# Kernel optimization log

Measured on AMD Instinct MI355X. Metric: run time of the kernel, lower is better.

Reference implementation:

```python
import jax, jax.numpy as jnp
import numpy as np

N = 100000
E = 1600000
IN, H, OUT = 128, 128, 64


def setup_inputs() -> dict:
    key = jax.random.key(0)
    k1, k2, k3, k4, k5, k6 = jax.random.split(key, 6)
    x = jax.random.normal(k1, (N, IN), dtype=jnp.float32)
    edge_index = jax.random.randint(k2, (2, E), 0, N, dtype=jnp.int64)
    W1 = jax.random.normal(k3, (IN, H), dtype=jnp.float32) / np.sqrt(IN)
    b1 = jnp.zeros((H,), dtype=jnp.float32)
    W2 = jax.random.normal(k4, (H, OUT), dtype=jnp.float32) / np.sqrt(H)
    b2 = jnp.zeros((OUT,), dtype=jnp.float32)
    return {"x": x, "edge_index": edge_index, "W1": W1, "b1": b1, "W2": W2, "b2": b2}


def gcn_conv(x, src, dst, W, b, num_nodes):
    # PyG GCNConv: linear transform, then symmetric-normalized aggregation
    h = x @ W                                         # (N, d_out)
    ones = jnp.ones(src.shape[0], dtype=h.dtype)
    deg = jax.ops.segment_sum(ones, dst, num_segments=num_nodes)  # in-degree incl. self-loops
    dis = jax.lax.rsqrt(jnp.maximum(deg, 1.0))        # deg >= 1 due to self-loops
    norm = dis[src] * dis[dst]                        # (E+N,)
    msg = h[src] * norm[:, None]                      # gather + scale (memory-bound)
    out = jax.ops.segment_sum(msg, dst, num_segments=num_nodes)
    return out + b


def reference(x, edge_index, W1, b1, W2, b2):
    loop = jnp.arange(N, dtype=edge_index.dtype)
    src = jnp.concatenate([edge_index[0], loop])
    dst = jnp.concatenate([edge_index[1], loop])
    h = gcn_conv(x, src, dst, W1, b1, N)
    h = jax.nn.relu(h)                                # dropout: eval mode (identity)
    out = gcn_conv(h, src, dst, W2, b2, N)
    return jax.nn.sigmoid(out) * 0.8 + 0.1
```

## Files before the change

kernel.cpp:

```cpp
#include <hip/hip_runtime.h>
#include <cstdint>
#include <cstddef>

#define IN_F 128
#define HID  128
#define OUTF 64

typedef unsigned int   uint32;
typedef unsigned short ushort16;

using frag_ab = __attribute__((ext_vector_type(8))) short;
using frag_cd = __attribute__((ext_vector_type(4))) float;

static constexpr int TPB = 256;
static constexpr int PT_TILE = 2048;
static constexpr int PT_EPT  = 8;
static constexpr int MAXBK   = 512;

__device__ __forceinline__ float bflo(uint32 u) { return __uint_as_float(u << 16); }
__device__ __forceinline__ float bfhi(uint32 u) { return __uint_as_float(u & 0xFFFF0000u); }
__device__ __forceinline__ ushort16 f2bf(float f) {
    uint32 x = __float_as_uint(f);
    x = (x + 0x7FFFu + ((x >> 16) & 1u)) >> 16;
    return (ushort16)x;
}
__device__ __forceinline__ uint32 packbf(float a, float b) {
    return (uint32)f2bf(a) | ((uint32)f2bf(b) << 16);
}

__global__ void detect_i64_kernel(const uint32* __restrict__ p, int npairs, int* __restrict__ flag) {
    __shared__ int anynz;
    if (threadIdx.x == 0) anynz = 0;
    __syncthreads();
    int i = threadIdx.x;
    if (i < npairs && p[2 * i + 1] != 0u) atomicOr(&anynz, 1);
    __syncthreads();
    if (threadIdx.x == 0) *flag = (anynz == 0) ? 1 : 0;
}

__device__ __forceinline__ int load_idx(const void* p, int i, bool i64) {
    return i64 ? (int)((const long long*)p)[i] : ((const int*)p)[i];
}

__global__ __launch_bounds__(256) void partition_kernel(
    const void* __restrict__ ei, int E, const int* __restrict__ flag,
    int nbuckets, int bcap,
    int* __restrict__ bcur, uint32* __restrict__ bbuf)
{
    __shared__ uint32   stash[PT_TILE];
    __shared__ ushort16 bidx[PT_TILE];
    __shared__ int hist[MAXBK];
    __shared__ int scanb[MAXBK];
    __shared__ int gbase[MAXBK];
    __shared__ int sum256[256];

    bool i64 = (*flag != 0);
    int tile0 = blockIdx.x * PT_TILE;
    int tid = threadIdx.x;

    for (int i = tid; i < nbuckets; i += 256) hist[i] = 0;
    __syncthreads();

    uint32 pck[PT_EPT];
    int    lofs[PT_EPT];
    short  bkt[PT_EPT];
#pragma unroll
    for (int j = 0; j < PT_EPT; ++j) {
        int e = tile0 + j * 256 + tid;
        if (e < E) {
            int s = load_idx(ei, e, i64);
            int d = load_idx(ei, E + e, i64);
            int b = d >> 8;
            pck[j]  = (uint32)s | ((uint32)(d & 255) << 24);
            bkt[j]  = (short)b;
            lofs[j] = atomicAdd(&hist[b], 1);
        } else bkt[j] = -1;
    }
    __syncthreads();

    for (int i = tid; i < nbuckets; i += 256)
        gbase[i] = hist[i] ? atomicAdd(&bcur[i], hist[i]) : 0;

    {
        int lt = tid * 2;
        int h0 = 0, h1 = 0;
        if (lt + 0 < nbuckets) h0 = hist[lt + 0];
        if (lt + 1 < nbuckets) h1 = hist[lt + 1];
        int lsum = h0 + h1;
        sum256[tid] = lsum;
        __syncthreads();
        for (int off = 1; off < 256; off <<= 1) {
            int t = (tid >= off) ? sum256[tid - off] : 0;
            __syncthreads();
            sum256[tid] += t;
            __syncthreads();
        }
        int excl = sum256[tid] - lsum;
        if (lt + 0 < nbuckets) scanb[lt + 0] = excl;
        if (lt + 1 < nbuckets) scanb[lt + 1] = excl + h0;
    }
    __syncthreads();

#pragma unroll
    for (int j = 0; j < PT_EPT; ++j) {
        if (bkt[j] >= 0) {
            int p = scanb[bkt[j]] + lofs[j];
            stash[p] = pck[j];
            bidx[p]  = (ushort16)bkt[j];
        }
    }
    __syncthreads();

    int total = min(PT_TILE, E - tile0);
    for (int k = tid; k < total; k += 256) {
        int b = bidx[k];
        int dst = gbase[b] + (k - scanb[b]);
        if (dst < bcap) bbuf[(size_t)b * bcap + dst] = stash[k];
    }
}

__global__ __launch_bounds__(256) void bucket_count_kernel(
    const uint32* __restrict__ bbuf, const int* __restrict__ bcur,
    int* __restrict__ counts, float* __restrict__ dis, int N, int bcap)
{
    __shared__ int h[256];
    int tid = threadIdx.x;
    h[tid] = 0;
    __syncthreads();
    int b = blockIdx.x;
    int cnt = min(bcur[b], bcap);
    const uint32* src = bbuf + (size_t)b * bcap;
    for (int k = tid; k < cnt; k += 256) atomicAdd(&h[src[k] >> 24], 1);
    __syncthreads();
    int node = (b << 8) + tid;
    if (node < N) {
        int c = h[tid];
        counts[node] = c;
        dis[node] = rsqrtf((float)(c + 1));
    }
}

__global__ __launch_bounds__(256) void bucket_fill_kernel(
    const uint32* __restrict__ bbuf, const int* __restrict__ bcur,
    const int* __restrict__ row_ptr, int* __restrict__ csr, int N, int bcap)
{
    __shared__ int cur[256];
    int b = blockIdx.x;
    int node = (b << 8) + threadIdx.x;
    cur[threadIdx.x] = (node < N) ? row_ptr[node] : 0;
    __syncthreads();
    int cnt = min(bcur[b], bcap);
    const uint32* src = bbuf + (size_t)b * bcap;
    for (int k = threadIdx.x; k < cnt; k += 256) {
        uint32 p = src[k];
        int dl = p >> 24;
        int pos = atomicAdd(&cur[dl], 1);
        csr[pos] = (int)(p & 0xFFFFFF);
    }
}

__global__ void hist_kernel(const void* __restrict__ ei, int E, const int* __restrict__ flag,
                            int* __restrict__ counts) {
    int e = blockIdx.x * TPB + threadIdx.x;
    if (e >= E) return;
    bool i64 = (*flag != 0);
    atomicAdd(&counts[load_idx(ei, E + e, i64)], 1);
}

__global__ void fill_kernel(const void* __restrict__ ei, int E, const int* __restrict__ flag,
                            int* __restrict__ cursor, int* __restrict__ csr_src) {
    int e = blockIdx.x * TPB + threadIdx.x;
    if (e >= E) return;
    bool i64 = (*flag != 0);
    int s = load_idx(ei, e, i64);
    int d = load_idx(ei, E + e, i64);
    int pos = atomicAdd(&cursor[d], 1);
    csr_src[pos] = s;
}

__global__ void dis_kernel(const int* __restrict__ counts, float* __restrict__ dis, int n) {
    int i = blockIdx.x * TPB + threadIdx.x;
    if (i < n) dis[i] = rsqrtf((float)(counts[i] + 1));
}

__global__ void scan_block_kernel(const int* __restrict__ counts, int* __restrict__ excl,
                                  int* __restrict__ partials, int n) {
    __shared__ int tmp[TPB];
    int tid = threadIdx.x, gid = blockIdx.x * TPB + tid;
    int v = (gid < n) ? counts[gid] : 0;
    tmp[tid] = v;
    __syncthreads();
    for (int off = 1; off < TPB; off <<= 1) {
        int t = (tid >= off) ? tmp[tid - off] : 0;
        __syncthreads();
        tmp[tid] += t;
        __syncthreads();
    }
    if (gid < n) excl[gid] = tmp[tid] - v;
    if (tid == TPB - 1) partials[blockIdx.x] = tmp[TPB - 1];
}

__global__ void scan_partials_kernel(int* __restrict__ partials, int nb) {
    __shared__ int tmp[512];
    int tid = threadIdx.x;
    int v = (tid < nb) ? partials[tid] : 0;
    tmp[tid] = v;
    __syncthreads();
    for (int off = 1; off < 512; off <<= 1) {
        int t = (tid >= off) ? tmp[tid - off] : 0;
        __syncthreads();
        tmp[tid] += t;
        __syncthreads();
    }
    if (tid < nb) partials[tid] = tmp[tid] - v;
}

__global__ void add_offsets_kernel(int* __restrict__ excl, const int* __restrict__ partials,
                                   int* __restrict__ cursor, int n) {
    int i = blockIdx.x * TPB + threadIdx.x;
    if (i < n) {
        int v = excl[i] + partials[blockIdx.x];
        excl[i] = v;
        cursor[i] = v;
    }
}

template <int C, bool XBF>
__global__ __launch_bounds__(256) void gemm_mfma_kernel(
    const void* __restrict__ Xv, const float* __restrict__ W,
    const float* __restrict__ dis, ushort16* __restrict__ out, int M)
{
    constexpr int NB = C / 16;
    __shared__ ushort16 Wt[C][136];

    for (int i = threadIdx.x; i < 128 * C; i += 256) {
        int k = i / C, c = i % C;
        Wt[c][k] = f2bf(W[i]);
    }
    __syncthreads();

    int wid  = threadIdx.x >> 6;
    int lane = threadIdx.x & 63;
    int g    = lane >> 4;
    int li   = lane & 15;

    int row = blockIdx.x * 64 + wid * 16 + li;
    int rc  = min(row, M - 1);

    frag_cd acc[NB];
#pragma unroll
    for (int i = 0; i < NB; ++i) acc[i] = (frag_cd)0.0f;

#pragma unroll
    for (int t = 0; t < 4; ++t) {
        frag_ab a;
        if (XBF) {
            const ushort16* xp = (const ushort16*)Xv + (size_t)rc * 128 + t * 32 + g * 8;
            a = *(const frag_ab*)xp;
        } else {
            const float* xp = (const float*)Xv + (size_t)rc * 128 + t * 32 + g * 8;
            float4 p = *(const float4*)xp;
            float4 q = *(const float4*)(xp + 4);
            a[0] = (short)f2bf(p.x); a[1] = (short)f2bf(p.y);
            a[2] = (short)f2bf(p.z); a[3] = (short)f2bf(p.w);
            a[4] = (short)f2bf(q.x); a[5] = (short)f2bf(q.y);
            a[6] = (short)f2bf(q.z); a[7] = (short)f2bf(q.w);
        }
#pragma unroll
        for (int cb = 0; cb < NB; ++cb) {
            frag_ab b = *(const frag_ab*)&Wt[cb * 16 + li][t * 32 + g * 8];
            acc[cb] = __builtin_amdgcn_mfma_f32_16x16x32_bf16(a, b, acc[cb], 0, 0, 0);
        }
    }

    int ro = blockIdx.x * 64 + wid * 16 + g * 4;
#pragma unroll
    for (int r = 0; r < 4; ++r) {
        int rr = ro + r;
        if (rr < M) {
            float dsc = dis[rr];
#pragma unroll
            for (int cb = 0; cb < NB; ++cb)
                out[(size_t)rr * C + cb * 16 + li] = f2bf(acc[cb][r] * dsc);
        }
    }
}

__global__ __launch_bounds__(256) void agg128_kernel(
    const uint32* __restrict__ hs, const int* __restrict__ csr,
    const int* __restrict__ row_ptr, const int* __restrict__ counts,
    const float* __restrict__ dis, const float* __restrict__ b,
    uint32* __restrict__ out, int n)
{
    int wave = threadIdx.x >> 6;
    int lane = threadIdx.x & 63;
    int g    = lane >> 4;
    int sl   = lane & 15;
    int node = blockIdx.x * 4 + wave;
    if (node >= n) return;

    const uint4* hsv = (const uint4*)hs;
    float a0 = 0.f, a1 = 0.f, a2 = 0.f, a3 = 0.f,
          a4 = 0.f, a5 = 0.f, a6 = 0.f, a7 = 0.f;
    if (g == 0) {
        uint4 u = hsv[(size_t)node * 16 + sl];
        a0 = bflo(u.x); a1 = bfhi(u.x); a2 = bflo(u.y); a3 = bfhi(u.y);
        a4 = bflo(u.z); a5 = bfhi(u.z); a6 = bflo(u.w); a7 = bfhi(u.w);
    }

    int start = row_ptr[node];
    int end   = start + counts[node];
    int k = start;
    for (; k + 15 < end; k += 16) {
        int base = k + (g << 2);
        int s0 = csr[base], s1 = csr[base + 1], s2 = csr[base + 2], s3 = csr[base + 3];
        uint4 u0 = hsv[(size_t)s0 * 16 + sl];
        uint4 u1 = hsv[(size_t)s1 * 16 + sl];
        uint4 u2 = hsv[(size_t)s2 * 16 + sl];
        uint4 u3 = hsv[(size_t)s3 * 16 + sl];
        a0 += bflo(u0.x) + bflo(u1.x) + bflo(u2.x) + bflo(u3.x);
        a1 += bfhi(u0.x) + bfhi(u1.x) + bfhi(u2.x) + bfhi(u3.x);
        a2 += bflo(u0.y) + bflo(u1.y) + bflo(u2.y) + bflo(u3.y);
        a3 += bfhi(u0.y) + bfhi(u1.y) + bfhi(u2.y) + bfhi(u3.y);
        a4 += bflo(u0.z) + bflo(u1.z) + bflo(u2.z) + bflo(u3.z);
        a5 += bfhi(u0.z) + bfhi(u1.z) + bfhi(u2.z) + bfhi(u3.z);
        a6 += bflo(u0.w) + bflo(u1.w) + bflo(u2.w) + bflo(u3.w);
        a7 += bfhi(u0.w) + bfhi(u1.w) + bfhi(u2.w) + bfhi(u3.w);
    }
    for (; k + 7 < end; k += 8) {
        int base = k + (g << 1);
        int s0 = csr[base], s1 = csr[base + 1];
        uint4 u0 = hsv[(size_t)s0 * 16 + sl];
        uint4 u1 = hsv[(size_t)s1 * 16 + sl];
        a0 += bflo(u0.x) + bflo(u1.x);  a1 += bfhi(u0.x) + bfhi(u1.x);
        a2 += bflo(u0.y) + bflo(u1.y);  a3 += bfhi(u0.y) + bfhi(u1.y);
        a4 += bflo(u0.z) + bflo(u1.z);  a5 += bfhi(u0.z) + bfhi(u1.z);
        a6 += bflo(u0.w) + bflo(u1.w);  a7 += bfhi(u0.w) + bfhi(u1.w);
    }
    for (; k < end; k += 4) {
        int e = k + g;
        if (e < end) {
            uint4 u = hsv[(size_t)csr[e] * 16 + sl];
            a0 += bflo(u.x); a1 += bfhi(u.x); a2 += bflo(u.y); a3 += bfhi(u.y);
            a4 += bflo(u.z); a5 += bfhi(u.z); a6 += bflo(u.w); a7 += bfhi(u.w);
        }
    }

    a0 += __shfl_xor(a0, 16, 64); a0 += __shfl_xor(a0, 32, 64);
    a1 += __shfl_xor(a1, 16, 64); a1 += __shfl_xor(a1, 32, 64);
    a2 += __shfl_xor(a2, 16, 64); a2 += __shfl_xor(a2, 32, 64);
    a3 += __shfl_xor(a3, 16, 64); a3 += __shfl_xor(a3, 32, 64);
    a4 += __shfl_xor(a4, 16, 64); a4 += __shfl_xor(a4, 32, 64);
    a5 += __shfl_xor(a5, 16, 64); a5 += __shfl_xor(a5, 32, 64);
    a6 += __shfl_xor(a6, 16, 64); a6 += __shfl_xor(a6, 32, 64);
    a7 += __shfl_xor(a7, 16, 64); a7 += __shfl_xor(a7, 32, 64);

    if (g == 0) {
        float dsc = dis[node];
        float4 bb0 = ((const float4*)b)[sl * 2];
        float4 bb1 = ((const float4*)b)[sl * 2 + 1];
        float v0 = fmaxf(a0 * dsc + bb0.x, 0.0f);
        float v1 = fmaxf(a1 * dsc + bb0.y, 0.0f);
        float v2 = fmaxf(a2 * dsc + bb0.z, 0.0f);
        float v3 = fmaxf(a3 * dsc + bb0.w, 0.0f);
        float v4 = fmaxf(a4 * dsc + bb1.x, 0.0f);
        float v5 = fmaxf(a5 * dsc + bb1.y, 0.0f);
        float v6 = fmaxf(a6 * dsc + bb1.z, 0.0f);
        float v7 = fmaxf(a7 * dsc + bb1.w, 0.0f);
        uint4 o;
        o.x = packbf(v0, v1); o.y = packbf(v2, v3);
        o.z = packbf(v4, v5); o.w = packbf(v6, v7);
        ((uint4*)out)[(size_t)node * 16 + sl] = o;
    }
}

__global__ __launch_bounds__(256) void agg64_kernel(
    const uint32* __restrict__ hs, const int* __restrict__ csr,
    const int* __restrict__ row_ptr, const int* __restrict__ counts,
    const float* __restrict__ dis, const float* __restrict__ b,
    float* __restrict__ out, int n)
{
    int wave = threadIdx.x >> 6;
    int lane = threadIdx.x & 63;
    int g    = lane >> 3;
    int sl   = lane & 7;
    int node = blockIdx.x * 4 + wave;
    if (node >= n) return;

    const uint4* hsv = (const uint4*)hs;
    float a0 = 0.f, a1 = 0.f, a2 = 0.f, a3 = 0.f,
          a4 = 0.f, a5 = 0.f, a6 = 0.f, a7 = 0.f;
    if (g == 0) {
        uint4 u = hsv[(size_t)node * 8 + sl];
        a0 = bflo(u.x); a1 = bfhi(u.x); a2 = bflo(u.y); a3 = bfhi(u.y);
        a4 = bflo(u.z); a5 = bfhi(u.z); a6 = bflo(u.w); a7 = bfhi(u.w);
    }

    int start = row_ptr[node];
    int end   = start + counts[node];
    int k = start;
    for (; k + 15 < end; k += 16) {
        int base = k + (g << 1);
        int s0 = csr[base], s1 = csr[base + 1];
        uint4 u0 = hsv[(size_t)s0 * 8 + sl];
        uint4 u1 = hsv[(size_t)s1 * 8 + sl];
        a0 += bflo(u0.x) + bflo(u1.x);  a1 += bfhi(u0.x) + bfhi(u1.x);
        a2 += bflo(u0.y) + bflo(u1.y);  a3 += bfhi(u0.y) + bfhi(u1.y);
        a4 += bflo(u0.z) + bflo(u1.z);  a5 += bfhi(u0.z) + bfhi(u1.z);
        a6 += bflo(u0.w) + bflo(u1.w);  a7 += bfhi(u0.w) + bfhi(u1.w);
    }
    for (; k + 7 < end; k += 8) {
        int e = k + g;
        uint4 u = hsv[(size_t)csr[e] * 8 + sl];
        a0 += bflo(u.x); a1 += bfhi(u.x); a2 += bflo(u.y); a3 += bfhi(u.y);
        a4 += bflo(u.z); a5 += bfhi(u.z); a6 += bflo(u.w); a7 += bfhi(u.w);
    }
    for (; k < end; k += 8) {
        int e = k + g;
        if (e < end) {
            uint4 u = hsv[(size_t)csr[e] * 8 + sl];
            a0 += bflo(u.x); a1 += bfhi(u.x); a2 += bflo(u.y); a3 += bfhi(u.y);
            a4 += bflo(u.z); a5 += bfhi(u.z); a6 += bflo(u.w); a7 += bfhi(u.w);
        }
    }

    a0 += __shfl_xor(a0, 8, 64); a0 += __shfl_xor(a0, 16, 64); a0 += __shfl_xor(a0, 32, 64);
    a1 += __shfl_xor(a1, 8, 64); a1 += __shfl_xor(a1, 16, 64); a1 += __shfl_xor(a1, 32, 64);
    a2 += __shfl_xor(a2, 8, 64); a2 += __shfl_xor(a2, 16, 64); a2 += __shfl_xor(a2, 32, 64);
    a3 += __shfl_xor(a3, 8, 64); a3 += __shfl_xor(a3, 16, 64); a3 += __shfl_xor(a3, 32, 64);
    a4 += __shfl_xor(a4, 8, 64); a4 += __shfl_xor(a4, 16, 64); a4 += __shfl_xor(a4, 32, 64);
    a5 += __shfl_xor(a5, 8, 64); a5 += __shfl_xor(a5, 16, 64); a5 += __shfl_xor(a5, 32, 64);
    a6 += __shfl_xor(a6, 8, 64); a6 += __shfl_xor(a6, 16, 64); a6 += __shfl_xor(a6, 32, 64);
    a7 += __shfl_xor(a7, 8, 64); a7 += __shfl_xor(a7, 16, 64); a7 += __shfl_xor(a7, 32, 64);

    if (g == 0) {
        float dsc = dis[node];
        float4 bb0 = ((const float4*)b)[sl * 2];
        float4 bb1 = ((const float4*)b)[sl * 2 + 1];
        float4 o0, o1;
        o0.x = 0.1f + 0.8f / (1.0f + __expf(-(a0 * dsc + bb0.x)));
        o0.y = 0.1f + 0.8f / (1.0f + __expf(-(a1 * dsc + bb0.y)));
        o0.z = 0.1f + 0.8f / (1.0f + __expf(-(a2 * dsc + bb0.z)));
        o0.w = 0.1f + 0.8f / (1.0f + __expf(-(a3 * dsc + bb0.w)));
        o1.x = 0.1f + 0.8f / (1.0f + __expf(-(a4 * dsc + bb1.x)));
        o1.y = 0.1f + 0.8f / (1.0f + __expf(-(a5 * dsc + bb1.y)));
        o1.z = 0.1f + 0.8f / (1.0f + __expf(-(a6 * dsc + bb1.z)));
        o1.w = 0.1f + 0.8f / (1.0f + __expf(-(a7 * dsc + bb1.w)));
        ((float4*)out)[(size_t)node * 16 + sl * 2]     = o0;
        ((float4*)out)[(size_t)node * 16 + sl * 2 + 1] = o1;
    }
}

extern "C" void kernel_launch(void* const* d_in, const int* in_sizes, int n_in,
                              void* d_out, int out_size, void* d_ws, size_t ws_size,
                              hipStream_t stream) {
    const float* x  = (const float*)d_in[0];
    const void*  ei = d_in[1];
    const float* W1 = (const float*)d_in[2];
    const float* b1 = (const float*)d_in[3];
    const float* W2 = (const float*)d_in[4];
    const float* b2 = (const float*)d_in[5];

    const int N = in_sizes[0] / IN_F;
    const int E = in_sizes[1] / 2;

    const int nbuckets = (N + 255) >> 8;
    const int bcap     = (int)(2 * ((long long)E / (nbuckets > 0 ? nbuckets : 1)) + 2048);
    const bool bucketed = (nbuckets <= MAXBK);

    auto alignup = [](size_t v) { return (v + 255) & ~(size_t)255; };
    char* w = (char*)d_ws;
    size_t off = 0;
    int*      flag     = (int*)(w + off);      off = alignup(off + 16);
    int*      counts   = (int*)(w + off);      off = alignup(off + (size_t)(N + MAXBK) * sizeof(int));
    int*      bcur     = counts + N;
    int*      cursor   = (int*)(w + off);      off = alignup(off + (size_t)N * sizeof(int));
    int*      row_ptr  = (int*)(w + off);      off = alignup(off + (size_t)N * sizeof(int));
    int*      partials = (int*)(w + off);      off = alignup(off + 512 * sizeof(int));
    float*    dis      = (float*)(w + off);    off = alignup(off + (size_t)N * sizeof(float));
    int*      csr      = (int*)(w + off);      off = alignup(off + (size_t)E * sizeof(int));
    uint32*   bbuf     = (uint32*)(w + off);   off = alignup(off + (size_t)nbuckets * bcap * sizeof(uint32));
    uint32*   A        = (uint32*)(w + off);   off = alignup(off + (size_t)N * HID * sizeof(ushort16));
    uint32*   B        = (uint32*)(w + off);   off = alignup(off + (size_t)N * HID * sizeof(ushort16));

    const int nbN = (N + TPB - 1) / TPB;
    const int nbE = (E + TPB - 1) / TPB;

    detect_i64_kernel<<<1, TPB, 0, stream>>>((const uint32*)ei, 256, flag);
    hipMemsetAsync(counts, 0, (size_t)(N + MAXBK) * sizeof(int), stream);

    if (bucketed) {
        partition_kernel<<<(E + PT_TILE - 1) / PT_TILE, TPB, 0, stream>>>(
            ei, E, flag, nbuckets, bcap, bcur, bbuf);
        bucket_count_kernel<<<nbuckets, TPB, 0, stream>>>(bbuf, bcur, counts, dis, N, bcap);
        scan_block_kernel<<<nbN, TPB, 0, stream>>>(counts, row_ptr, partials, N);
        scan_partials_kernel<<<1, 512, 0, stream>>>(partials, nbN);
        add_offsets_kernel<<<nbN, TPB, 0, stream>>>(row_ptr, partials, cursor, N);
        bucket_fill_kernel<<<nbuckets, TPB, 0, stream>>>(bbuf, bcur, row_ptr, csr, N, bcap);
    } else {
        hist_kernel<<<nbE, TPB, 0, stream>>>(ei, E, flag, counts);
        dis_kernel<<<nbN, TPB, 0, stream>>>(counts, dis, N);
        scan_block_kernel<<<nbN, TPB, 0, stream>>>(counts, row_ptr, partials, N);
        scan_partials_kernel<<<1, 512, 0, stream>>>(partials, nbN);
        add_offsets_kernel<<<nbN, TPB, 0, stream>>>(row_ptr, partials, cursor, N);
        fill_kernel<<<nbE, TPB, 0, stream>>>(ei, E, flag, cursor, csr);
    }

    const int gemmBlocks = (N + 63) / 64;

    gemm_mfma_kernel<HID, false><<<gemmBlocks, TPB, 0, stream>>>(x, W1, dis, (ushort16*)A, N);
    agg128_kernel<<<(N + 3) / 4, TPB, 0, stream>>>(A, csr, row_ptr, counts, dis, b1, B, N);

    gemm_mfma_kernel<OUTF, true><<<gemmBlocks, TPB, 0, stream>>>(B, W2, dis, (ushort16*)A, N);
    agg64_kernel<<<(N + 3) / 4, TPB, 0, stream>>>(A, csr, row_ptr, counts, dis, b2, (float*)d_out, N);
}
```

Baseline: 209.7 us.

## Fuse edge partition with first GEMM in one launch and fold row_ptr scan

The edge partitioning and the first-layer GEMM now run in one kernel launch, with the block index choosing the work, so the two independent stages can overlap. To make that possible, the GEMM no longer applies the source degree scaling. Instead, agg128 gathers dis[src] for every edge and scales each message with an FMA. The global three-kernel scan for row_ptr is replaced by a per-bucket base scan plus an in-block scan inside the count kernel, and the memset now clears only the bucket cursors. The cost is an extra dis gather per edge in the first aggregation and a larger shared-memory footprint for the fused kernel.

```diff
diff --git a/kernel.cpp b/kernel.cpp
--- a/kernel.cpp
+++ b/kernel.cpp
@@ -16,6 +16,7 @@
 static constexpr int PT_TILE = 2048;
 static constexpr int PT_EPT  = 8;
 static constexpr int MAXBK   = 512;
+static constexpr int MEGA_SMEM = 34816;
 
 __device__ __forceinline__ float bflo(uint32 u) { return __uint_as_float(u << 16); }
 __device__ __forceinline__ float bfhi(uint32 u) { return __uint_as_float(u & 0xFFFF0000u); }
@@ -42,19 +43,17 @@
     return i64 ? (int)((const long long*)p)[i] : ((const int*)p)[i];
 }
 
-__global__ __launch_bounds__(256) void partition_kernel(
-    const void* __restrict__ ei, int E, const int* __restrict__ flag,
-    int nbuckets, int bcap,
-    int* __restrict__ bcur, uint32* __restrict__ bbuf)
-{
-    __shared__ uint32   stash[PT_TILE];
-    __shared__ ushort16 bidx[PT_TILE];
-    __shared__ int hist[MAXBK];
-    __shared__ int scanb[MAXBK];
-    __shared__ int gbase[MAXBK];
-    __shared__ int sum256[256];
-
-    bool i64 = (*flag != 0);
+__device__ void partition_body(char* smem, const void* __restrict__ ei, int E, bool i64,
+                               int nbuckets, int bcap,
+                               int* __restrict__ bcur, uint32* __restrict__ bbuf)
+{
+    uint32*   stash  = (uint32*)smem;
+    ushort16* bidx   = (ushort16*)(smem + 8192);
+    int*      hist   = (int*)(smem + 12288);
+    int*      scanb  = (int*)(smem + 14336);
+    int*      gbase  = (int*)(smem + 16384);
+    int*      sum256 = (int*)(smem + 18432);
+
     int tile0 = blockIdx.x * PT_TILE;
     int tid = threadIdx.x;
 
@@ -119,11 +118,96 @@
     }
 }
 
-__global__ __launch_bounds__(256) void bucket_count_kernel(
-    const uint32* __restrict__ bbuf, const int* __restrict__ bcur,
-    int* __restrict__ counts, float* __restrict__ dis, int N, int bcap)
+__device__ void gemm1_body(char* smem, int gb, const float* __restrict__ X,
+                           const float* __restrict__ W, ushort16* __restrict__ out, int M)
+{
+    typedef ushort16 WtRow[136];
+    WtRow* Wt = (WtRow*)smem;
+
+    for (int i = threadIdx.x; i < 128 * 128; i += 256) {
+        int k = i >> 7, c = i & 127;
+        Wt[c][k] = f2bf(W[i]);
+    }
+    __syncthreads();
+
+    int wid  = threadIdx.x >> 6;
+    int lane = threadIdx.x & 63;
+    int g    = lane >> 4;
+    int li   = lane & 15;
+
+    int row = gb * 64 + wid * 16 + li;
+    int rc  = min(row, M - 1);
+
+    frag_cd acc[8];
+#pragma unroll
+    for (int i = 0; i < 8; ++i) acc[i] = (frag_cd)0.0f;
+
+#pragma unroll
+    for (int t = 0; t < 4; ++t) {
+        const float* xp = X + (size_t)rc * 128 + t * 32 + g * 8;
+        float4 p = *(const float4*)xp;
+        float4 q = *(const float4*)(xp + 4);
+        frag_ab a;
+        a[0] = (short)f2bf(p.x); a[1] = (short)f2bf(p.y);
+        a[2] = (short)f2bf(p.z); a[3] = (short)f2bf(p.w);
+        a[4] = (short)f2bf(q.x); a[5] = (short)f2bf(q.y);
+        a[6] = (short)f2bf(q.z); a[7] = (short)f2bf(q.w);
+#pragma unroll
+        for (int cb = 0; cb < 8; ++cb) {
+            frag_ab b = *(const frag_ab*)&Wt[cb * 16 + li][t * 32 + g * 8];
+            acc[cb] = __builtin_amdgcn_mfma_f32_16x16x32_bf16(a, b, acc[cb], 0, 0, 0);
+        }
+    }
+
+    int ro = gb * 64 + wid * 16 + g * 4;
+#pragma unroll
+    for (int r = 0; r < 4; ++r) {
+        int rr = ro + r;
+        if (rr < M) {
+#pragma unroll
+            for (int cb = 0; cb < 8; ++cb)
+                out[(size_t)rr * 128 + cb * 16 + li] = f2bf(acc[cb][r]);
+        }
+    }
+}
+
+__global__ __launch_bounds__(256) void mega1_kernel(
+    const void* __restrict__ ei, int E, const int* __restrict__ flag,
+    int nbuckets, int bcap, int* __restrict__ bcur, uint32* __restrict__ bbuf,
+    const float* __restrict__ X, const float* __restrict__ W1,
+    ushort16* __restrict__ H, int M, int PB)
+{
+    __shared__ char smem[MEGA_SMEM];
+    if ((int)blockIdx.x < PB) {
+        partition_body(smem, ei, E, (*flag != 0), nbuckets, bcap, bcur, bbuf);
+    } else {
+        gemm1_body(smem, blockIdx.x - PB, X, W1, H, M);
+    }
+}
+
+__global__ void bucket_base_kernel(const int* __restrict__ bcur, int* __restrict__ bbase,
+                                   int nbuckets, int bcap) {
+    __shared__ int tmp[512];
+    int tid = threadIdx.x;
+    int v = (tid < nbuckets) ? min(bcur[tid], bcap) : 0;
+    tmp[tid] = v;
+    __syncthreads();
+    for (int off = 1; off < 512; off <<= 1) {
+        int t = (tid >= off) ? tmp[tid - off] : 0;
+        __syncthreads();
+        tmp[tid] += t;
+        __syncthreads();
+    }
+    if (tid < nbuckets) bbase[tid] = tmp[tid] - v;
+}
+
+__global__ __launch_bounds__(256) void bucket_count2_kernel(
+    const uint32* __restrict__ bbuf, const int* __restrict__ bcur, const int* __restrict__ bbase,
+    int* __restrict__ counts, float* __restrict__ dis, int* __restrict__ row_ptr,
+    int N, int bcap)
 {
     __shared__ int h[256];
+    __shared__ int sc[256];
     int tid = threadIdx.x;
     h[tid] = 0;
     __syncthreads();
@@ -132,11 +216,20 @@
     const uint32* src = bbuf + (size_t)b * bcap;
     for (int k = tid; k < cnt; k += 256) atomicAdd(&h[src[k] >> 24], 1);
     __syncthreads();
+    int v = h[tid];
+    sc[tid] = v;
+    __syncthreads();
+    for (int off = 1; off < 256; off <<= 1) {
+        int t = (tid >= off) ? sc[tid - off] : 0;
+        __syncthreads();
+        sc[tid] += t;
+        __syncthreads();
+    }
     int node = (b << 8) + tid;
     if (node < N) {
-        int c = h[tid];
-        counts[node] = c;
-        dis[node] = rsqrtf((float)(c + 1));
+        counts[node]  = v;
+        dis[node]     = rsqrtf((float)(v + 1));
+        row_ptr[node] = bbase[b] + sc[tid] - v;
     }
 }
 
@@ -225,7 +318,7 @@
     }
 }
 
-template <int C, bool XBF>
+template <int C, bool XBF, bool SCALE>
 __global__ __launch_bounds__(256) void gemm_mfma_kernel(
     const void* __restrict__ Xv, const float* __restrict__ W,
     const float* __restrict__ dis, ushort16* __restrict__ out, int M)
@@ -278,13 +371,19 @@
     for (int r = 0; r < 4; ++r) {
         int rr = ro + r;
         if (rr < M) {
-            float dsc = dis[rr];
+            float dsc = SCALE ? dis[rr] : 1.0f;
 #pragma unroll
             for (int cb = 0; cb < NB; ++cb)
                 out[(size_t)rr * C + cb * 16 + li] = f2bf(acc[cb][r] * dsc);
         }
     }
 }
+
+#define ACC8(u, d) \
+    a0 = fmaf(d, bflo(u.x), a0); a1 = fmaf(d, bfhi(u.x), a1); \
+    a2 = fmaf(d, bflo(u.y), a2); a3 = fmaf(d, bfhi(u.y), a3); \
+    a4 = fmaf(d, bflo(u.z), a4); a5 = fmaf(d, bfhi(u.z), a5); \
+    a6 = fmaf(d, bflo(u.w), a6); a7 = fmaf(d, bfhi(u.w), a7);
 
 __global__ __launch_bounds__(256) void agg128_kernel(
     const uint32* __restrict__ hs, const int* __restrict__ csr,
@@ -300,12 +399,12 @@
     if (node >= n) return;
 
     const uint4* hsv = (const uint4*)hs;
+    float dsc = dis[node];
     float a0 = 0.f, a1 = 0.f, a2 = 0.f, a3 = 0.f,
           a4 = 0.f, a5 = 0.f, a6 = 0.f, a7 = 0.f;
     if (g == 0) {
         uint4 u = hsv[(size_t)node * 16 + sl];
-        a0 = bflo(u.x); a1 = bfhi(u.x); a2 = bflo(u.y); a3 = bfhi(u.y);
-        a4 = bflo(u.z); a5 = bfhi(u.z); a6 = bflo(u.w); a7 = bfhi(u.w);
+        ACC8(u, dsc);
     }
 
     int start = row_ptr[node];
@@ -314,35 +413,28 @@
     for (; k + 15 < end; k += 16) {
         int base = k + (g << 2);
         int s0 = csr[base], s1 = csr[base + 1], s2 = csr[base + 2], s3 = csr[base + 3];
+        float d0 = dis[s0], d1 = dis[s1], d2 = dis[s2], d3 = dis[s3];
         uint4 u0 = hsv[(size_t)s0 * 16 + sl];
         uint4 u1 = hsv[(size_t)s1 * 16 + sl];
         uint4 u2 = hsv[(size_t)s2 * 16 + sl];
         uint4 u3 = hsv[(size_t)s3 * 16 + sl];
-        a0 += bflo(u0.x) + bflo(u1.x) + bflo(u2.x) + bflo(u3.x);
-        a1 += bfhi(u0.x) + bfhi(u1.x) + bfhi(u2.x) + bfhi(u3.x);
-        a2 += bflo(u0.y) + bflo(u1.y) + bflo(u2.y) + bflo(u3.y);
-        a3 += bfhi(u0.y) + bfhi(u1.y) + bfhi(u2.y) + bfhi(u3.y);
-        a4 += bflo(u0.z) + bflo(u1.z) + bflo(u2.z) + bflo(u3.z);
-        a5 += bfhi(u0.z) + bfhi(u1.z) + bfhi(u2.z) + bfhi(u3.z);
-        a6 += bflo(u0.w) + bflo(u1.w) + bflo(u2.w) + bflo(u3.w);
-        a7 += bfhi(u0.w) + bfhi(u1.w) + bfhi(u2.w) + bfhi(u3.w);
+        ACC8(u0, d0); ACC8(u1, d1); ACC8(u2, d2); ACC8(u3, d3);
     }
     for (; k + 7 < end; k += 8) {
         int base = k + (g << 1);
         int s0 = csr[base], s1 = csr[base + 1];
+        float d0 = dis[s0], d1 = dis[s1];
         uint4 u0 = hsv[(size_t)s0 * 16 + sl];
         uint4 u1 = hsv[(size_t)s1 * 16 + sl];
-        a0 += bflo(u0.x) + bflo(u1.x);  a1 += bfhi(u0.x) + bfhi(u1.x);
-        a2 += bflo(u0.y) + bflo(u1.y);  a3 += bfhi(u0.y) + bfhi(u1.y);
-        a4 += bflo(u0.z) + bflo(u1.z);  a5 += bfhi(u0.z) + bfhi(u1.z);
-        a6 += bflo(u0.w) + bflo(u1.w);  a7 += bfhi(u0.w) + bfhi(u1.w);
+        ACC8(u0, d0); ACC8(u1, d1);
     }
     for (; k < end; k += 4) {
         int e = k + g;
         if (e < end) {
-            uint4 u = hsv[(size_t)csr[e] * 16 + sl];
-            a0 += bflo(u.x); a1 += bfhi(u.x); a2 += bflo(u.y); a3 += bfhi(u.y);
-            a4 += bflo(u.z); a5 += bfhi(u.z); a6 += bflo(u.w); a7 += bfhi(u.w);
+            int s0 = csr[e];
+            float d0 = dis[s0];
+            uint4 u = hsv[(size_t)s0 * 16 + sl];
+            ACC8(u, d0);
         }
     }
 
@@ -356,7 +448,6 @@
     a7 += __shfl_xor(a7, 16, 64); a7 += __shfl_xor(a7, 32, 64);
 
     if (g == 0) {
-        float dsc = dis[node];
         float4 bb0 = ((const float4*)b)[sl * 2];
         float4 bb1 = ((const float4*)b)[sl * 2 + 1];
         float v0 = fmaxf(a0 * dsc + bb0.x, 0.0f);
@@ -392,8 +483,7 @@
           a4 = 0.f, a5 = 0.f, a6 = 0.f, a7 = 0.f;
     if (g == 0) {
         uint4 u = hsv[(size_t)node * 8 + sl];
-        a0 = bflo(u.x); a1 = bfhi(u.x); a2 = bflo(u.y); a3 = bfhi(u.y);
-        a4 = bflo(u.z); a5 = bfhi(u.z); a6 = bflo(u.w); a7 = bfhi(u.w);
+        ACC8(u, 1.0f);
     }
 
     int start = row_ptr[node];
@@ -404,23 +494,18 @@
         int s0 = csr[base], s1 = csr[base + 1];
         uint4 u0 = hsv[(size_t)s0 * 8 + sl];
         uint4 u1 = hsv[(size_t)s1 * 8 + sl];
-        a0 += bflo(u0.x) + bflo(u1.x);  a1 += bfhi(u0.x) + bfhi(u1.x);
-        a2 += bflo(u0.y) + bflo(u1.y);  a3 += bfhi(u0.y) + bfhi(u1.y);
-        a4 += bflo(u0.z) + bflo(u1.z);  a5 += bfhi(u0.z) + bfhi(u1.z);
-        a6 += bflo(u0.w) + bflo(u1.w);  a7 += bfhi(u0.w) + bfhi(u1.w);
+        ACC8(u0, 1.0f); ACC8(u1, 1.0f);
     }
     for (; k + 7 < end; k += 8) {
         int e = k + g;
         uint4 u = hsv[(size_t)csr[e] * 8 + sl];
-        a0 += bflo(u.x); a1 += bfhi(u.x); a2 += bflo(u.y); a3 += bfhi(u.y);
-        a4 += bflo(u.z); a5 += bfhi(u.z); a6 += bflo(u.w); a7 += bfhi(u.w);
+        ACC8(u, 1.0f);
     }
     for (; k < end; k += 8) {
         int e = k + g;
         if (e < end) {
             uint4 u = hsv[(size_t)csr[e] * 8 + sl];
-            a0 += bflo(u.x); a1 += bfhi(u.x); a2 += bflo(u.y); a3 += bfhi(u.y);
-            a4 += bflo(u.z); a5 += bfhi(u.z); a6 += bflo(u.w); a7 += bfhi(u.w);
+            ACC8(u, 1.0f);
         }
     }
 
@@ -474,6 +559,7 @@
     int*      flag     = (int*)(w + off);      off = alignup(off + 16);
     int*      counts   = (int*)(w + off);      off = alignup(off + (size_t)(N + MAXBK) * sizeof(int));
     int*      bcur     = counts + N;
+    int*      bbase    = (int*)(w + off);      off = alignup(off + MAXBK * sizeof(int));
     int*      cursor   = (int*)(w + off);      off = alignup(off + (size_t)N * sizeof(int));
     int*      row_ptr  = (int*)(w + off);      off = alignup(off + (size_t)N * sizeof(int));
     int*      partials = (int*)(w + off);      off = alignup(off + 512 * sizeof(int));
@@ -485,32 +571,31 @@
 
     const int nbN = (N + TPB - 1) / TPB;
     const int nbE = (E + TPB - 1) / TPB;
+    const int gemmBlocks = (N + 63) / 64;
 
     detect_i64_kernel<<<1, TPB, 0, stream>>>((const uint32*)ei, 256, flag);
-    hipMemsetAsync(counts, 0, (size_t)(N + MAXBK) * sizeof(int), stream);
 
     if (bucketed) {
-        partition_kernel<<<(E + PT_TILE - 1) / PT_TILE, TPB, 0, stream>>>(
-            ei, E, flag, nbuckets, bcap, bcur, bbuf);
-        bucket_count_kernel<<<nbuckets, TPB, 0, stream>>>(bbuf, bcur, counts, dis, N, bcap);
-        scan_block_kernel<<<nbN, TPB, 0, stream>>>(counts, row_ptr, partials, N);
-        scan_partials_kernel<<<1, 512, 0, stream>>>(partials, nbN);
-        add_offsets_kernel<<<nbN, TPB, 0, stream>>>(row_ptr, partials, cursor, N);
+        hipMemsetAsync(bcur, 0, MAXBK * sizeof(int), stream);
+        const int PB = (E + PT_TILE - 1) / PT_TILE;
+        mega1_kernel<<<PB + gemmBlocks, TPB, 0, stream>>>(
+            ei, E, flag, nbuckets, bcap, bcur, bbuf, x, W1, (ushort16*)A, N, PB);
+        bucket_base_kernel<<<1, 512, 0, stream>>>(bcur, bbase, nbuckets, bcap);
+        bucket_count2_kernel<<<nbuckets, TPB, 0, stream>>>(bbuf, bcur, bbase, counts, dis, row_ptr, N, bcap);
         bucket_fill_kernel<<<nbuckets, TPB, 0, stream>>>(bbuf, bcur, row_ptr, csr, N, bcap);
     } else {
+        hipMemsetAsync(counts, 0, (size_t)(N + MAXBK) * sizeof(int), stream);
         hist_kernel<<<nbE, TPB, 0, stream>>>(ei, E, flag, counts);
         dis_kernel<<<nbN, TPB, 0, stream>>>(counts, dis, N);
         scan_block_kernel<<<nbN, TPB, 0, stream>>>(counts, row_ptr, partials, N);
         scan_partials_kernel<<<1, 512, 0, stream>>>(partials, nbN);
         add_offsets_kernel<<<nbN, TPB, 0, stream>>>(row_ptr, partials, cursor, N);
         fill_kernel<<<nbE, TPB, 0, stream>>>(ei, E, flag, cursor, csr);
-    }
-
-    const int gemmBlocks = (N + 63) / 64;
-
-    gemm_mfma_kernel<HID, false><<<gemmBlocks, TPB, 0, stream>>>(x, W1, dis, (ushort16*)A, N);
+        gemm_mfma_kernel<HID, false, false><<<gemmBlocks, TPB, 0, stream>>>(x, W1, dis, (ushort16*)A, N);
+    }
+
     agg128_kernel<<<(N + 3) / 4, TPB, 0, stream>>>(A, csr, row_ptr, counts, dis, b1, B, N);
 
-    gemm_mfma_kernel<OUTF, true><<<gemmBlocks, TPB, 0, stream>>>(B, W2, dis, (ushort16*)A, N);
+    gemm_mfma_kernel<OUTF, true, true><<<gemmBlocks, TPB, 0, stream>>>(B, W2, dis, (ushort16*)A, N);
     agg64_kernel<<<(N + 3) / 4, TPB, 0, stream>>>(A, csr, row_ptr, counts, dis, b2, (float*)d_out, N);
 }
```

Result: faster. 203.3 us (-3.1%).
